# Kernel optimization log

Hardware: AMD Instinct MI355X
Metric: run time of the kernel (lower is better)

## Reference

```python
import jax, jax.numpy as jnp
import numpy as np

B, D, H = 65536, 256, 16

def setup_inputs() -> dict:
    key = jax.random.key(0)
    k_x, k_w1, k_b1, k_w2, k_b2 = jax.random.split(key, 5)
    # per-feature subnet params: Linear(1,H) -> tanh -> Linear(H,1)
    # torch default init: U(-1/sqrt(fan_in), 1/sqrt(fan_in))
    w1 = jax.random.uniform(k_w1, (D, H), jnp.float32, -1.0, 1.0)          # fan_in=1
    b1 = jax.random.uniform(k_b1, (D, H), jnp.float32, -1.0, 1.0)
    bnd = 1.0 / np.sqrt(H)
    w2 = jax.random.uniform(k_w2, (D, H), jnp.float32, -bnd, bnd)          # fan_in=H
    b2 = jax.random.uniform(k_b2, (D,), jnp.float32, -bnd, bnd)
    x = jax.random.normal(k_x, (B, D), jnp.float32)
    return {"x": x, "w1": w1, "b1": b1, "w2": w2, "b2": b2}

def reference(x, w1, b1, w2, b2) -> jnp.ndarray:
    # h[b,d,h] = tanh(x[b,d]*w1[d,h] + b1[d,h])
    h = jnp.tanh(x[:, :, None] * w1[None, :, :] + b1[None, :, :])
    # out[b] = sum_d ( h[b,d,:] . w2[d,:] + b2[d] )
    out = jnp.einsum('bdh,dh->b', h, w2) + jnp.sum(b2)
    return out[:, None]  # [B, 1] to match torch output shape
```

## Files before the change

kernel.cpp:

```cpp
#include <hip/hip_runtime.h>
#include <hip/hip_fp16.h>
#include <cstdint>

#define B_TOT  65536
#define D_TOT  256
#define H_SUB  16

#define TBL_N      512
#define TBL_XMIN   (-8.0f)
#define TBL_RANGE  16.0f
#define TBL_DELTA  (TBL_RANGE / (float)TBL_N)
#define INV_DELTA  ((float)TBL_N / TBL_RANGE)
#define T_OFF      (-(TBL_XMIN) * INV_DELTA)

#define DG      32
#define NG      (D_TOT / DG)
#define BCHUNK  1024
#define NTH     256

__device__ __forceinline__ float tanh_fast(float z) {
    float e = __builtin_amdgcn_exp2f(z * 2.8853900817779268f);
    return 1.0f - 2.0f * __builtin_amdgcn_rcpf(e + 1.0f);
}

__global__ void build_tables(const float* __restrict__ w1,
                             const float* __restrict__ b1,
                             const float* __restrict__ w2,
                             const float* __restrict__ b2,
                             uint32_t* __restrict__ tab) {
    int gid = blockIdx.x * NTH + threadIdx.x;
    int d = gid >> 9;
    int i = gid & (TBL_N - 1);
    float x0 = TBL_XMIN + (float)i * TBL_DELTA;
    float x1 = x0 + TBL_DELTA;
    float f0 = 0.0f, f1 = 0.0f;
#pragma unroll
    for (int h = 0; h < H_SUB; ++h) {
        float a = w1[d * H_SUB + h];
        float c = b1[d * H_SUB + h];
        float w = w2[d * H_SUB + h];
        f0 += w * tanh_fast(fmaf(a, x0, c));
        f1 += w * tanh_fast(fmaf(a, x1, c));
    }
    float val = f0 + b2[d];
    float slp = f1 - f0;
    __half2 h2 = __halves2half2(__float2half_rn(val), __float2half_rn(slp));
    tab[gid] = *reinterpret_cast<uint32_t*>(&h2);
}

__global__ __launch_bounds__(NTH, 2) void kan_forward(
        const float* __restrict__ x,
        const uint32_t* __restrict__ tab,
        float* __restrict__ out) {
    __shared__ uint32_t sT[DG * TBL_N];

    const int g  = blockIdx.x & (NG - 1);
    const int bc = blockIdx.x >> 3;

    {
        const uint4* src = reinterpret_cast<const uint4*>(tab + g * DG * TBL_N);
        uint4* dst = reinterpret_cast<uint4*>(sT);
#pragma unroll
        for (int k = 0; k < (DG * TBL_N / 4) / NTH; ++k)
            dst[threadIdx.x + k * NTH] = src[threadIdx.x + k * NTH];
    }
    __syncthreads();

    const int b0 = bc * BCHUNK + threadIdx.x;
#pragma unroll
    for (int bi = 0; bi < BCHUNK / NTH; ++bi) {
        const int b = b0 + bi * NTH;
        const float4* xr =
            reinterpret_cast<const float4*>(x + (size_t)b * D_TOT + g * DG);
        float acc = 0.0f;
#pragma unroll
        for (int j = 0; j < DG / 4; ++j) {
            float4 xv = xr[j];
            float vv[4] = {xv.x, xv.y, xv.z, xv.w};
#pragma unroll
            for (int c = 0; c < 4; ++c) {
                float t = fmaf(vv[c], INV_DELTA, T_OFF);
                t = fminf(fmaxf(t, 0.0f), (float)(TBL_N - 1));
                float fi = floorf(t);
                float u = t - fi;
                uint32_t e = sT[(j * 4 + c) * TBL_N + (int)fi];
                union { uint32_t u32; __half2 h2; } cvt;
                cvt.u32 = e;
                acc += fmaf(__high2float(cvt.h2), u, __low2float(cvt.h2));
            }
        }
        atomicAdd(&out[b], acc);
    }
}

extern "C" void kernel_launch(void* const* d_in, const int* in_sizes, int n_in,
                              void* d_out, int out_size, void* d_ws, size_t ws_size,
                              hipStream_t stream) {
    const float* x  = (const float*)d_in[0];
    const float* w1 = (const float*)d_in[1];
    const float* b1 = (const float*)d_in[2];
    const float* w2 = (const float*)d_in[3];
    const float* b2 = (const float*)d_in[4];
    float* out = (float*)d_out;
    uint32_t* tab = (uint32_t*)d_ws;

    hipMemsetAsync(d_out, 0, (size_t)out_size * sizeof(float), stream);

    build_tables<<<dim3(D_TOT * TBL_N / NTH), dim3(NTH), 0, stream>>>(
        w1, b1, w2, b2, tab);

    kan_forward<<<dim3((B_TOT / BCHUNK) * NG), dim3(NTH), 0, stream>>>(
        x, tab, out);
}
```

Before: 108.7 us.

## Halve lookup table, coalesce x reads with per-row lane groups, fuse output zeroing

Table resolution drops from 512 to 256 entries per feature, halving the shared-memory table to 32KB so more blocks fit per CU (launch bounds raised to 4). The forward loop is reorganised so 8 lanes share one row, each reading a float4 of that row's 32-feature slice, giving coalesced 128-byte row segments; partial sums are reduced with xor shuffles before one atomic per row. The output memset is folded into the table-build kernel, removing a separate launch. Coarser table spacing adds interpolation error, which is the accuracy risk taken on.

```diff
diff --git a/kernel.cpp b/kernel.cpp
--- a/kernel.cpp
+++ b/kernel.cpp
@@ -6,16 +6,15 @@
 #define D_TOT  256
 #define H_SUB  16
 
-#define TBL_N      512
+#define TBL_N      256
 #define TBL_XMIN   (-8.0f)
-#define TBL_RANGE  16.0f
-#define TBL_DELTA  (TBL_RANGE / (float)TBL_N)
-#define INV_DELTA  ((float)TBL_N / TBL_RANGE)
-#define T_OFF      (-(TBL_XMIN) * INV_DELTA)
+#define TBL_DELTA  0.0625f
+#define INV_DELTA  16.0f
+#define T_OFF      128.0f
 
 #define DG      32
 #define NG      (D_TOT / DG)
-#define BCHUNK  1024
+#define RPB     512
 #define NTH     256
 
 __device__ __forceinline__ float tanh_fast(float z) {
@@ -27,9 +26,11 @@
                              const float* __restrict__ b1,
                              const float* __restrict__ w2,
                              const float* __restrict__ b2,
-                             uint32_t* __restrict__ tab) {
+                             uint32_t* __restrict__ tab,
+                             float* __restrict__ out) {
     int gid = blockIdx.x * NTH + threadIdx.x;
-    int d = gid >> 9;
+    out[gid] = 0.0f;
+    int d = gid >> 8;
     int i = gid & (TBL_N - 1);
     float x0 = TBL_XMIN + (float)i * TBL_DELTA;
     float x1 = x0 + TBL_DELTA;
@@ -48,7 +49,7 @@
     tab[gid] = *reinterpret_cast<uint32_t*>(&h2);
 }
 
-__global__ __launch_bounds__(NTH, 2) void kan_forward(
+__global__ __launch_bounds__(NTH, 4) void kan_forward(
         const float* __restrict__ x,
         const uint32_t* __restrict__ tab,
         float* __restrict__ out) {
@@ -66,30 +67,36 @@
     }
     __syncthreads();
 
-    const int b0 = bc * BCHUNK + threadIdx.x;
-#pragma unroll
-    for (int bi = 0; bi < BCHUNK / NTH; ++bi) {
-        const int b = b0 + bi * NTH;
-        const float4* xr =
-            reinterpret_cast<const float4*>(x + (size_t)b * D_TOT + g * DG);
+    const int lane   = threadIdx.x & 63;
+    const int wave   = threadIdx.x >> 6;
+    const int subrow = lane >> 3;
+    const int fq     = lane & 7;
+
+    const int row0 = bc * RPB + wave * 8 + subrow;
+    const float* xb = x + (size_t)row0 * D_TOT + g * DG + fq * 4;
+
+#pragma unroll 4
+    for (int it = 0; it < RPB / 32; ++it) {
+        const float4 xv =
+            *reinterpret_cast<const float4*>(xb + (size_t)it * 32 * D_TOT);
+        float xs[4] = {xv.x, xv.y, xv.z, xv.w};
         float acc = 0.0f;
 #pragma unroll
-        for (int j = 0; j < DG / 4; ++j) {
-            float4 xv = xr[j];
-            float vv[4] = {xv.x, xv.y, xv.z, xv.w};
-#pragma unroll
-            for (int c = 0; c < 4; ++c) {
-                float t = fmaf(vv[c], INV_DELTA, T_OFF);
-                t = fminf(fmaxf(t, 0.0f), (float)(TBL_N - 1));
-                float fi = floorf(t);
-                float u = t - fi;
-                uint32_t e = sT[(j * 4 + c) * TBL_N + (int)fi];
-                union { uint32_t u32; __half2 h2; } cvt;
-                cvt.u32 = e;
-                acc += fmaf(__high2float(cvt.h2), u, __low2float(cvt.h2));
-            }
+        for (int c = 0; c < 4; ++c) {
+            float t = fmaf(xs[c], INV_DELTA, T_OFF);
+            t = fminf(fmaxf(t, 0.0f), 255.99f);
+            float fi = floorf(t);
+            float u = t - fi;
+            uint32_t e = sT[(fq * 4 + c) * TBL_N + (int)fi];
+            union { uint32_t u32; __half2 h2; } cv;
+            cv.u32 = e;
+            acc += fmaf(__high2float(cv.h2), u, __low2float(cv.h2));
         }
-        atomicAdd(&out[b], acc);
+        acc += __shfl_xor(acc, 1);
+        acc += __shfl_xor(acc, 2);
+        acc += __shfl_xor(acc, 4);
+        if (fq == 0)
+            atomicAdd(&out[row0 + it * 32], acc);
     }
 }
 
@@ -104,11 +111,9 @@
     float* out = (float*)d_out;
     uint32_t* tab = (uint32_t*)d_ws;
 
-    hipMemsetAsync(d_out, 0, (size_t)out_size * sizeof(float), stream);
+    build_tables<<<dim3(D_TOT * TBL_N / NTH), dim3(NTH), 0, stream>>>(
+        w1, b1, w2, b2, tab, out);
 
-    build_tables<<<dim3(D_TOT * TBL_N / NTH), dim3(NTH), 0, stream>>>(
-        w1, b1, w2, b2, tab);
-
-    kan_forward<<<dim3((B_TOT / BCHUNK) * NG), dim3(NTH), 0, stream>>>(
+    kan_forward<<<dim3((B_TOT / RPB) * NG), dim3(NTH), 0, stream>>>(
         x, tab, out);
 }
```

Measured after the change: 109.1 us. Within noise of the previous version (+0.4%).
